# Performance work log

Measured on AMD Instinct MI355X. Metric: run time of the kernel, lower is better.

## Reference

```python
import jax, jax.numpy as jnp
import numpy as np

N_NODES = 50000
N_EDGES = 800000
EPS = 1e-5


def _glorot(key, fan_in, fan_out):
    lim = np.sqrt(6.0 / (fan_in + fan_out))
    return jax.random.uniform(key, (fan_in, fan_out), jnp.float32, -lim, lim)


def setup_inputs() -> dict:
    key = jax.random.key(0)
    ks = jax.random.split(key, 16)
    x = jax.random.normal(ks[0], (N_NODES, 88), jnp.float32)
    edge_index = jax.random.randint(ks[1], (2, N_EDGES), 0, N_NODES, jnp.int64)
    dims = [(88, 70), (70, 60), (60, 50), (50, 60), (60, 70), (70, 88)]
    inp = {"x": x, "edge_index": edge_index}
    for i, (fi, fo) in enumerate(dims):
        inp[f"W{i+1}"] = _glorot(ks[2 + i], fi, fo)
        inp[f"b{i+1}"] = jnp.zeros((fo,), jnp.float32)
    # BatchNorm affine params for layers with bn: widths 70,60,60,70
    for i, w in enumerate([70, 60, 60, 70]):
        inp[f"g{i+1}"] = jnp.ones((w,), jnp.float32)
        inp[f"be{i+1}"] = jnp.zeros((w,), jnp.float32)
    return inp


def _gcn_norm(edge_index, n_nodes):
    # add self-loops, symmetric normalization: D^-1/2 (A+I) D^-1/2
    loop = jnp.arange(n_nodes, dtype=edge_index.dtype)
    src = jnp.concatenate([edge_index[0], loop])
    dst = jnp.concatenate([edge_index[1], loop])
    deg = jax.ops.segment_sum(jnp.ones_like(dst, jnp.float32), dst, num_segments=n_nodes)
    dis = jnp.where(deg > 0, jax.lax.rsqrt(deg), 0.0)
    norm = dis[src] * dis[dst]  # [E+N]
    return src, dst, norm


def _gcn(x, W, b, src, dst, norm, n_nodes):
    h = x @ W  # transform first (small out dim)
    msg = h[src] * norm[:, None]
    return jax.ops.segment_sum(msg, dst, num_segments=n_nodes) + b


def _bn(x, g, be):
    mu = jnp.mean(x, axis=0)
    var = jnp.mean(jnp.square(x - mu), axis=0)
    return g * (x - mu) * jax.lax.rsqrt(var + EPS) + be


def reference(x, edge_index, W1, b1, W2, b2, W3, b3, W4, b4, W5, b5, W6, b6,
              g1, be1, g2, be2, g3, be3, g4, be4):
    n = x.shape[0]
    src, dst, norm = _gcn_norm(edge_index, n)
    # encoder
    h = jax.nn.relu(_gcn(x, W1, b1, src, dst, norm, n))
    h = _bn(h, g1, be1)
    h = jax.nn.relu(_gcn(h, W2, b2, src, dst, norm, n))
    h = _bn(h, g2, be2)
    h = _gcn(h, W3, b3, src, dst, norm, n)
    # decoder
    h = jax.nn.relu(_gcn(h, W4, b4, src, dst, norm, n))
    h = _bn(h, g3, be3)
    h = jax.nn.relu(_gcn(h, W5, b5, src, dst, norm, n))
    h = _bn(h, g4, be4)
    h = _gcn(h, W6, b6, src, dst, norm, n)
    return h
```

## Files before the change

### kernel.cpp

```cpp
#include <hip/hip_runtime.h>
#include <hip/hip_bf16.h>

typedef unsigned int  uint_t;
typedef unsigned short ushort_t;

#define NN 50000
#define NE 800000
#define NBLK 196

static inline int cdiv(long long a, long long b) { return (int)((a + b - 1) / b); }

__device__ inline float bflo(uint_t u) { return __uint_as_float(u << 16); }
__device__ inline float bfhi(uint_t u) { return __uint_as_float(u & 0xffff0000u); }
__device__ inline uint_t packbf(float x, float y) {
    uint_t xu = __float_as_uint(x), yu = __float_as_uint(y);
    xu += 0x7fffu + ((xu >> 16) & 1u);
    yu += 0x7fffu + ((yu >> 16) & 1u);
    return (xu >> 16) | (yu & 0xffff0000u);
}
__device__ inline ushort_t packbf1(float x) {
    uint_t xu = __float_as_uint(x);
    xu += 0x7fffu + ((xu >> 16) & 1u);
    return (ushort_t)(xu >> 16);
}


__global__ void k_prep(int* __restrict__ deg, float* __restrict__ bnacc) {
    int i = blockIdx.x * blockDim.x + threadIdx.x;
    if (i < NN) deg[i] = 0;
    if (i < 768) bnacc[i] = 0.0f;
}

__global__ void k_hist(const int* __restrict__ dst, int* __restrict__ deg) {
    int e = blockIdx.x * blockDim.x + threadIdx.x;
    if (e < NE) {
        int d = dst[e];
        if ((unsigned)d < NN) atomicAdd(&deg[d], 1);
    }
}

__global__ void k_bsum(const int* __restrict__ deg, int* __restrict__ bsum) {
    __shared__ int l[256];
    int tid = threadIdx.x;
    int i = blockIdx.x * 256 + tid;
    l[tid] = (i < NN) ? deg[i] : 0;
    __syncthreads();
    for (int o = 128; o > 0; o >>= 1) {
        if (tid < o) l[tid] += l[tid + o];
        __syncthreads();
    }
    if (tid == 0) bsum[blockIdx.x] = l[0];
}

__global__ void k_bscan(const int* __restrict__ bsum, int* __restrict__ boff,
                        int* __restrict__ row_ptr) {
    __shared__ int l[256];
    int tid = threadIdx.x;
    int v = (tid < NBLK) ? bsum[tid] : 0;
    l[tid] = v;
    __syncthreads();
    for (int o = 1; o < 256; o <<= 1) {
        int t = (tid >= o) ? l[tid - o] : 0;
        __syncthreads();
        l[tid] += t;
        __syncthreads();
    }
    boff[tid] = l[tid] - v;
    if (tid == 255) row_ptr[NN] = l[255];
}

__global__ void k_rowptr(const int* __restrict__ deg, const int* __restrict__ boff,
                         int* __restrict__ row_ptr, int* __restrict__ cursor,
                         float* __restrict__ dis) {
    __shared__ int l[256];
    int tid = threadIdx.x;
    int i = blockIdx.x * 256 + tid;
    int v = (i < NN) ? deg[i] : 0;
    l[tid] = v;
    __syncthreads();
    for (int o = 1; o < 256; o <<= 1) {
        int t = (tid >= o) ? l[tid - o] : 0;
        __syncthreads();
        l[tid] += t;
        __syncthreads();
    }
    if (i < NN) {
        int excl = boff[blockIdx.x] + l[tid] - v;
        row_ptr[i] = excl;
        cursor[i] = excl;
        dis[i] = rsqrtf((float)(v + 1));
    }
}

__global__ void k_fill(const int* __restrict__ src, const int* __restrict__ dst,
                       const float* __restrict__ dis,
                       int* __restrict__ cursor, int* __restrict__ col,
                       float* __restrict__ wgt) {
    int e = blockIdx.x * blockDim.x + threadIdx.x;
    if (e < NE) {
        int s = src[e], d = dst[e];
        if ((unsigned)s < NN && (unsigned)d < NN) {
            int p = atomicAdd(&cursor[d], 1);
            col[p] = s;
            wgt[p] = dis[s] * dis[d];
        }
    }
}

template<int FI, int FO, int IN_BN, int OUT_B>
__global__ void k_fold(const float* __restrict__ bnacc, const float* __restrict__ g,
                       const float* __restrict__ be, const float* __restrict__ b,
                       const float* __restrict__ W,
                       float* __restrict__ Wp, float* __restrict__ biasf) {
    constexpr int NT  = (FO + 15) / 16;
    constexpr int FOP = 16 * NT;
    __shared__ float scl[IN_BN ? FI : 1], shl[IN_BN ? FI : 1];
    int tid = threadIdx.x;
    if (IN_BN) {
        if (tid < FI) {
            const float inv_n = 1.0f / NN;
            float mu = bnacc[tid] * inv_n;
            float va = bnacc[96 + tid] * inv_n - mu * mu;
            float r  = rsqrtf(va + 1e-5f);
            float sc = g[tid] * r;
            scl[tid] = sc;
            shl[tid] = be[tid] - mu * sc;
        }
        __syncthreads();
    }
    for (int idx = tid; idx < FI * FOP; idx += 256) {
        int k = idx / FOP, j = idx - k * FOP;
        float w = (j < FO) ? W[k * FO + j] : 0.0f;
        if (IN_BN) w *= scl[k];
        Wp[(k >> 1) * 2 * FOP + 2 * j + (k & 1)] = w;
    }
    if (tid < FOP) {
        float a = (OUT_B && tid < FO) ? b[tid] : 0.0f;
        if (IN_BN && tid < FO) {
            #pragma unroll 4
            for (int k = 0; k < FI; ++k) a = fmaf(shl[k], W[k * FO + tid], a);
        }
        biasf[tid] = a;
    }
}

template<int FI, int FO, int IN_BN, int IN_F32, int OUT_F32>
__global__ __launch_bounds__(256)
void k_dense(const void* __restrict__ Xv, const float* __restrict__ Wp,
             const float* __restrict__ biasf, void* __restrict__ Hv) {
    constexpr int NT  = (FO + 15) / 16;
    constexpr int FOP = 16 * NT;
    constexpr int FIP = FI + 2;
    constexpr int KP  = FI / 2;

    __shared__ __align__(16) float xs[64 * FIP];

    int tid = threadIdx.x;
    int node0 = blockIdx.x * 64;

    if (IN_F32) {
        for (int idx = tid; idx < 64 * FI; idx += 256) {
            int r = idx / FI, c = idx - r * FI;
            int n = node0 + r;
            float v = (n < NN) ? ((const float*)Xv)[(size_t)n * FI + c] : 0.0f;
            if (IN_BN) v = fmaxf(v, 0.0f);
            xs[r * FIP + c] = v;
        }
    } else {
        for (int idx = tid; idx < 64 * KP; idx += 256) {
            int r = idx / KP, c2 = idx - r * KP;
            int n = node0 + r;
            uint_t u = (n < NN) ? ((const uint_t*)Xv)[(size_t)n * KP + c2] : 0u;
            float f0 = bflo(u), f1 = bfhi(u);
            if (IN_BN) { f0 = fmaxf(f0, 0.0f); f1 = fmaxf(f1, 0.0f); }
            xs[r * FIP + 2 * c2]     = f0;
            xs[r * FIP + 2 * c2 + 1] = f1;
        }
    }
    __syncthreads();

    int ng = tid >> 4;
    int cg = tid & 15;

    float acc[4][NT];
    #pragma unroll
    for (int i = 0; i < 4; ++i)
        #pragma unroll
        for (int t = 0; t < NT; ++t) acc[i][t] = biasf[cg + 16 * t];

    #pragma unroll 2
    for (int k = 0; k < FI; k += 2) {
        float2 xv[4];
        #pragma unroll
        for (int i = 0; i < 4; ++i)
            xv[i] = *(const float2*)&xs[(ng + 16 * i) * FIP + k];
        const float* wrow = &Wp[(k >> 1) * 2 * FOP];
        #pragma unroll
        for (int t = 0; t < NT; ++t) {
            float2 w = *(const float2*)&wrow[2 * (cg + 16 * t)];
            #pragma unroll
            for (int i = 0; i < 4; ++i)
                acc[i][t] = fmaf(xv[i].y, w.y, fmaf(xv[i].x, w.x, acc[i][t]));
        }
    }

    #pragma unroll
    for (int i = 0; i < 4; ++i) {
        int n = node0 + ng + 16 * i;
        if (n < NN) {
            #pragma unroll
            for (int t = 0; t < NT; ++t) {
                int j = cg + 16 * t;
                if (j < FO) {
                    if (OUT_F32) ((float*)Hv)[(size_t)n * FO + j] = acc[i][t];
                    else ((ushort_t*)Hv)[(size_t)n * FO + j] = packbf1(acc[i][t]);
                }
            }
        }
    }
}

template<int FO, int IN_BN, int OUT_BIAS>
__global__ void k_gather(const ushort_t* __restrict__ h, const int* __restrict__ row_ptr,
                         const int* __restrict__ col, const float* __restrict__ wgt,
                         const float* __restrict__ dis,
                         const float* __restrict__ bnacc, const float* __restrict__ g,
                         const float* __restrict__ be,
                         const float* __restrict__ b, ushort_t* __restrict__ A) {
    constexpr int F2 = FO / 2;
    int t = blockIdx.x * blockDim.x + threadIdx.x;
    if (t >= NN * F2) return;
    int i = t / F2;
    int j2 = t - i * F2;
    int j = 2 * j2;

    float sc0 = 1.0f, sh0 = 0.0f, sc1 = 1.0f, sh1 = 0.0f;
    if (IN_BN) {
        const float inv_n = 1.0f / NN;
        float mu0 = bnacc[j] * inv_n;
        float va0 = bnacc[96 + j] * inv_n - mu0 * mu0;
        float r0  = rsqrtf(va0 + 1e-5f);
        sc0 = g[j] * r0; sh0 = be[j] - mu0 * sc0;
        float mu1 = bnacc[j + 1] * inv_n;
        float va1 = bnacc[96 + j + 1] * inv_n - mu1 * mu1;
        float r1  = rsqrtf(va1 + 1e-5f);
        sc1 = g[j + 1] * r1; sh1 = be[j + 1] - mu1 * sc1;
    }

    const uint_t* h2 = (const uint_t*)h + j2;
    float di = dis[i];

    uint_t su = h2[(size_t)i * F2];
    float vx = bflo(su), vy = bfhi(su);
    if (IN_BN) { vx = fmaxf(vx, 0.0f) * sc0 + sh0; vy = fmaxf(vy, 0.0f) * sc1 + sh1; }
    float ax = vx * di * di;
    float ay = vy * di * di;

    int k = row_ptr[i], end = row_ptr[i + 1];
    for (; k + 8 <= end; k += 8) {
        uint_t uu[8]; float ww[8];
        #pragma unroll
        for (int q = 0; q < 8; ++q) {
            int s = col[k + q];
            ww[q] = wgt[k + q];
            uu[q] = h2[(size_t)s * F2];
        }
        #pragma unroll
        for (int q = 0; q < 8; ++q) {
            float tx = bflo(uu[q]), ty = bfhi(uu[q]);
            if (IN_BN) { tx = fmaxf(tx, 0.0f) * sc0 + sh0; ty = fmaxf(ty, 0.0f) * sc1 + sh1; }
            ax = fmaf(tx, ww[q], ax); ay = fmaf(ty, ww[q], ay);
        }
    }
    for (; k < end; ++k) {
        int s = col[k];
        float w = wgt[k];
        uint_t u = h2[(size_t)s * F2];
        float tx = bflo(u), ty = bfhi(u);
        if (IN_BN) { tx = fmaxf(tx, 0.0f) * sc0 + sh0; ty = fmaxf(ty, 0.0f) * sc1 + sh1; }
        ax = fmaf(tx, w, ax); ay = fmaf(ty, w, ay);
    }
    if (OUT_BIAS) { ax += b[j]; ay += b[j + 1]; }
    ((uint_t*)A)[(size_t)i * F2 + j2] = packbf(ax, ay);
}

template<int FO>
__global__ void k_bnpart(const ushort_t* __restrict__ A, float* __restrict__ acc) {
    constexpr int F2 = FO / 2;
    __shared__ float ls[96], lq[96];
    int tid = threadIdx.x;
    if (tid < 96) { ls[tid] = 0.0f; lq[tid] = 0.0f; }
    __syncthreads();
    const uint_t* A2 = (const uint_t*)A;
    int t2 = blockIdx.x * blockDim.x + tid;
    int j2 = t2 % F2;
    int stride = gridDim.x * blockDim.x;
    float sx = 0.0f, qx = 0.0f, sy = 0.0f, qy = 0.0f;
    for (; t2 < NN * F2; t2 += stride) {
        uint_t u = A2[t2];
        float x = fmaxf(bflo(u), 0.0f), y = fmaxf(bfhi(u), 0.0f);
        sx += x; qx += x * x;
        sy += y; qy += y * y;
    }
    atomicAdd(&ls[2 * j2], sx);     atomicAdd(&ls[2 * j2 + 1], sy);
    atomicAdd(&lq[2 * j2], qx);     atomicAdd(&lq[2 * j2 + 1], qy);
    __syncthreads();
    if (tid < FO) {
        atomicAdd(&acc[tid], ls[tid]);
        atomicAdd(&acc[96 + tid], lq[tid]);
    }
}

extern "C" void kernel_launch(void* const* d_in, const int* in_sizes, int n_in,
                              void* d_out, int out_size, void* d_ws, size_t ws_size,
                              hipStream_t stream) {
    const float* x = (const float*)d_in[0];
    const int* ei = (const int*)d_in[1];
    const int* src = ei;
    const int* dst = ei + NE;
    const float* W1 = (const float*)d_in[2];  const float* b1 = (const float*)d_in[3];
    const float* W2 = (const float*)d_in[4];  const float* b2 = (const float*)d_in[5];
    const float* W3 = (const float*)d_in[6];  const float* b3 = (const float*)d_in[7];
    const float* W4 = (const float*)d_in[8];  const float* b4 = (const float*)d_in[9];
    const float* W5 = (const float*)d_in[10]; const float* b5 = (const float*)d_in[11];
    const float* W6 = (const float*)d_in[12]; const float* b6 = (const float*)d_in[13];
    const float* g1 = (const float*)d_in[14]; const float* be1 = (const float*)d_in[15];
    const float* g2 = (const float*)d_in[16]; const float* be2 = (const float*)d_in[17];
    const float* g3 = (const float*)d_in[18]; const float* be3 = (const float*)d_in[19];
    const float* g4 = (const float*)d_in[20]; const float* be4 = (const float*)d_in[21];

    float* ws = (float*)d_ws;
    float* dis    = ws;
    float* bnacc  = dis + NN;
    float* Wp     = bnacc + 768;
    float* biasf  = Wp + 7040;
    float* wgt    = biasf + 96;
    int* deg      = (int*)(wgt + NE);
    int* row_ptr  = deg + NN;
    int* cursor   = row_ptr + NN + 1;
    int* col      = cursor + NN;
    int* bsum     = col + NE;
    int* boff     = bsum + 256;
    ushort_t* hB  = (ushort_t*)(boff + 256);
    ushort_t* aB  = hB + (size_t)NN * 70;
    float* out    = (float*)d_out;

    const int NB = 256;
    const int DGRID = cdiv(NN, 64);
    float* bn0 = bnacc;
    float* bn1 = bnacc + 192;
    float* bn2 = bnacc + 384;
    float* bn3 = bnacc + 576;

    k_prep<<<cdiv(NN, NB), NB, 0, stream>>>(deg, bnacc);
    k_hist<<<cdiv(NE, NB), NB, 0, stream>>>(dst, deg);
    k_bsum<<<NBLK, 256, 0, stream>>>(deg, bsum);
    k_bscan<<<1, 256, 0, stream>>>(bsum, boff, row_ptr);
    k_rowptr<<<NBLK, 256, 0, stream>>>(deg, boff, row_ptr, cursor, dis);
    k_fill<<<cdiv(NE, NB), NB, 0, stream>>>(src, dst, dis, cursor, col, wgt);

    k_fold<88, 70, 0, 0><<<1, 256, 0, stream>>>(nullptr, nullptr, nullptr, nullptr, W1, Wp, biasf);
    k_dense<88, 70, 0, 1, 0><<<DGRID, 256, 0, stream>>>(x, Wp, biasf, hB);
    k_gather<70, 0, 1><<<cdiv((long long)NN * 35, NB), NB, 0, stream>>>(
        hB, row_ptr, col, wgt, dis, nullptr, nullptr, nullptr, b1, aB);
    k_bnpart<70><<<35 * 56, NB, 0, stream>>>(aB, bn0);

    k_fold<70, 60, 1, 0><<<1, 256, 0, stream>>>(bn0, g1, be1, nullptr, W2, Wp, biasf);
    k_dense<70, 60, 1, 0, 0><<<DGRID, 256, 0, stream>>>(aB, Wp, biasf, hB);
    k_gather<60, 0, 1><<<cdiv((long long)NN * 30, NB), NB, 0, stream>>>(
        hB, row_ptr, col, wgt, dis, nullptr, nullptr, nullptr, b2, aB);
    k_bnpart<60><<<30 * 56, NB, 0, stream>>>(aB, bn1);

    k_fold<60, 50, 1, 0><<<1, 256, 0, stream>>>(bn1, g2, be2, nullptr, W3, Wp, biasf);
    k_dense<60, 50, 1, 0, 0><<<DGRID, 256, 0, stream>>>(aB, Wp, biasf, hB);
    k_gather<50, 0, 1><<<cdiv((long long)NN * 25, NB), NB, 0, stream>>>(
        hB, row_ptr, col, wgt, dis, nullptr, nullptr, nullptr, b3, aB);

    k_gather<50, 0, 0><<<cdiv((long long)NN * 25, NB), NB, 0, stream>>>(
        aB, row_ptr, col, wgt, dis, nullptr, nullptr, nullptr, nullptr, hB);
    k_fold<50, 60, 0, 1><<<1, 256, 0, stream>>>(nullptr, nullptr, nullptr, b4, W4, Wp, biasf);
    k_dense<50, 60, 0, 0, 0><<<DGRID, 256, 0, stream>>>(hB, Wp, biasf, aB);
    k_bnpart<60><<<30 * 56, NB, 0, stream>>>(aB, bn2);

    k_gather<60, 1, 0><<<cdiv((long long)NN * 30, NB), NB, 0, stream>>>(
        aB, row_ptr, col, wgt, dis, bn2, g3, be3, nullptr, hB);
    k_fold<60, 70, 0, 1><<<1, 256, 0, stream>>>(nullptr, nullptr, nullptr, b5, W5, Wp, biasf);
    k_dense<60, 70, 0, 0, 0><<<DGRID, 256, 0, stream>>>(hB, Wp, biasf, aB);
    k_bnpart<70><<<35 * 56, NB, 0, stream>>>(aB, bn3);

    k_gather<70, 1, 0><<<cdiv((long long)NN * 35, NB), NB, 0, stream>>>(
        aB, row_ptr, col, wgt, dis, bn3, g4, be4, nullptr, hB);
    k_fold<70, 88, 0, 1><<<1, 256, 0, stream>>>(nullptr, nullptr, nullptr, b6, W6, Wp, biasf);
    k_dense<70, 88, 0, 0, 1><<<DGRID, 256, 0, stream>>>(hB, Wp, biasf, out);
}
```

Before: 664.1 us.

## Fuse BN statistics into gather/dense, pack CSR col+weight, batch weight folds

Removes the separate k_bnpart passes by accumulating ReLU sum and sum-of-squares inside the gather or dense kernel that produces each activation. Column index and edge weight are packed into one int2 array so each edge needs a single load. The weight folds that do not depend on BN are batched into one multi-block launch at the start, and each layer gets its own Wp/bias slot. The gather becomes grid-stride with a fixed grid of 56*F2 blocks where stats are fused, which cuts parallelism and may add per-element overhead.

```diff
diff --git a/kernel.cpp b/kernel.cpp
--- a/kernel.cpp
+++ b/kernel.cpp
@@ -94,69 +94,77 @@
 
 __global__ void k_fill(const int* __restrict__ src, const int* __restrict__ dst,
                        const float* __restrict__ dis,
-                       int* __restrict__ cursor, int* __restrict__ col,
-                       float* __restrict__ wgt) {
+                       int* __restrict__ cursor, int2* __restrict__ cw) {
     int e = blockIdx.x * blockDim.x + threadIdx.x;
     if (e < NE) {
         int s = src[e], d = dst[e];
         if ((unsigned)s < NN && (unsigned)d < NN) {
             int p = atomicAdd(&cursor[d], 1);
-            col[p] = s;
-            wgt[p] = dis[s] * dis[d];
-        }
-    }
-}
-
-template<int FI, int FO, int IN_BN, int OUT_B>
-__global__ void k_fold(const float* __restrict__ bnacc, const float* __restrict__ g,
-                       const float* __restrict__ be, const float* __restrict__ b,
-                       const float* __restrict__ W,
-                       float* __restrict__ Wp, float* __restrict__ biasf) {
-    constexpr int NT  = (FO + 15) / 16;
-    constexpr int FOP = 16 * NT;
-    __shared__ float scl[IN_BN ? FI : 1], shl[IN_BN ? FI : 1];
-    int tid = threadIdx.x;
-    if (IN_BN) {
+            cw[p] = make_int2(s, __float_as_int(dis[s] * dis[d]));
+        }
+    }
+}
+
+struct FoldJob {
+    const float* W; const float* b;
+    const float* bnacc; const float* g; const float* be;
+    float* Wp; float* bf;
+    int FI, FO, in_bn, out_b;
+};
+struct FoldJobs { FoldJob j[4]; };
+
+__global__ void k_fold(FoldJobs jobs) {
+    FoldJob J = jobs.j[blockIdx.x];
+    const int FI = J.FI, FO = J.FO;
+    const int NT = (FO + 15) / 16, FOP = 16 * NT;
+    __shared__ float scl[96], shl[96];
+    int tid = threadIdx.x;
+    if (J.in_bn) {
         if (tid < FI) {
             const float inv_n = 1.0f / NN;
-            float mu = bnacc[tid] * inv_n;
-            float va = bnacc[96 + tid] * inv_n - mu * mu;
+            float mu = J.bnacc[tid] * inv_n;
+            float va = J.bnacc[96 + tid] * inv_n - mu * mu;
             float r  = rsqrtf(va + 1e-5f);
-            float sc = g[tid] * r;
+            float sc = J.g[tid] * r;
             scl[tid] = sc;
-            shl[tid] = be[tid] - mu * sc;
+            shl[tid] = J.be[tid] - mu * sc;
         }
         __syncthreads();
     }
     for (int idx = tid; idx < FI * FOP; idx += 256) {
         int k = idx / FOP, j = idx - k * FOP;
-        float w = (j < FO) ? W[k * FO + j] : 0.0f;
-        if (IN_BN) w *= scl[k];
-        Wp[(k >> 1) * 2 * FOP + 2 * j + (k & 1)] = w;
+        float w = (j < FO) ? J.W[k * FO + j] : 0.0f;
+        if (J.in_bn) w *= scl[k];
+        J.Wp[(k >> 1) * 2 * FOP + 2 * j + (k & 1)] = w;
     }
     if (tid < FOP) {
-        float a = (OUT_B && tid < FO) ? b[tid] : 0.0f;
-        if (IN_BN && tid < FO) {
-            #pragma unroll 4
-            for (int k = 0; k < FI; ++k) a = fmaf(shl[k], W[k * FO + tid], a);
-        }
-        biasf[tid] = a;
-    }
-}
-
-template<int FI, int FO, int IN_BN, int IN_F32, int OUT_F32>
+        float a = (J.out_b && tid < FO) ? J.b[tid] : 0.0f;
+        if (J.in_bn && tid < FO) {
+            for (int k = 0; k < FI; ++k) a = fmaf(shl[k], J.W[k * FO + tid], a);
+        }
+        J.bf[tid] = a;
+    }
+}
+
+template<int FI, int FO, int IN_BN, int IN_F32, int OUT_F32, int OUT_BN>
 __global__ __launch_bounds__(256)
 void k_dense(const void* __restrict__ Xv, const float* __restrict__ Wp,
-             const float* __restrict__ biasf, void* __restrict__ Hv) {
+             const float* __restrict__ biasf, void* __restrict__ Hv,
+             float* __restrict__ bnst) {
     constexpr int NT  = (FO + 15) / 16;
     constexpr int FOP = 16 * NT;
     constexpr int FIP = FI + 2;
     constexpr int KP  = FI / 2;
 
     __shared__ __align__(16) float xs[64 * FIP];
+    __shared__ float ls[96], lq[96];
 
     int tid = threadIdx.x;
     int node0 = blockIdx.x * 64;
+
+    if (OUT_BN) {
+        if (tid < 96) { ls[tid] = 0.0f; lq[tid] = 0.0f; }
+    }
 
     if (IN_F32) {
         for (int idx = tid; idx < 64 * FI; idx += 256) {
@@ -204,6 +212,27 @@
         }
     }
 
+    if (OUT_BN) {
+        #pragma unroll
+        for (int t = 0; t < NT; ++t) {
+            float ps = 0.0f, pq = 0.0f;
+            #pragma unroll
+            for (int i = 0; i < 4; ++i) {
+                if (node0 + ng + 16 * i < NN) {
+                    float r = fmaxf(acc[i][t], 0.0f);
+                    ps += r; pq += r * r;
+                }
+            }
+            atomicAdd(&ls[cg + 16 * t], ps);
+            atomicAdd(&lq[cg + 16 * t], pq);
+        }
+        __syncthreads();
+        if (tid < FO) {
+            atomicAdd(&bnst[tid], ls[tid]);
+            atomicAdd(&bnst[96 + tid], lq[tid]);
+        }
+    }
+
     #pragma unroll
     for (int i = 0; i < 4; ++i) {
         int n = node0 + ng + 16 * i;
@@ -220,18 +249,24 @@
     }
 }
 
-template<int FO, int IN_BN, int OUT_BIAS>
+template<int FO, int IN_BN, int OUT_BIAS, int OUT_BN>
 __global__ void k_gather(const ushort_t* __restrict__ h, const int* __restrict__ row_ptr,
-                         const int* __restrict__ col, const float* __restrict__ wgt,
-                         const float* __restrict__ dis,
+                         const int2* __restrict__ cw, const float* __restrict__ dis,
                          const float* __restrict__ bnacc, const float* __restrict__ g,
                          const float* __restrict__ be,
-                         const float* __restrict__ b, ushort_t* __restrict__ A) {
+                         const float* __restrict__ b, ushort_t* __restrict__ A,
+                         float* __restrict__ bnacc_out) {
     constexpr int F2 = FO / 2;
-    int t = blockIdx.x * blockDim.x + threadIdx.x;
-    if (t >= NN * F2) return;
-    int i = t / F2;
-    int j2 = t - i * F2;
+    __shared__ float ls[96], lq[96];
+    int tid = threadIdx.x;
+    if (OUT_BN) {
+        if (tid < 96) { ls[tid] = 0.0f; lq[tid] = 0.0f; }
+        __syncthreads();
+    }
+
+    int t0 = blockIdx.x * blockDim.x + tid;
+    const int stride = gridDim.x * blockDim.x;
+    int j2 = t0 % F2;
     int j = 2 * j2;
 
     float sc0 = 1.0f, sh0 = 0.0f, sc1 = 1.0f, sh1 = 0.0f;
@@ -248,66 +283,59 @@
     }
 
     const uint_t* h2 = (const uint_t*)h + j2;
-    float di = dis[i];
-
-    uint_t su = h2[(size_t)i * F2];
-    float vx = bflo(su), vy = bfhi(su);
-    if (IN_BN) { vx = fmaxf(vx, 0.0f) * sc0 + sh0; vy = fmaxf(vy, 0.0f) * sc1 + sh1; }
-    float ax = vx * di * di;
-    float ay = vy * di * di;
-
-    int k = row_ptr[i], end = row_ptr[i + 1];
-    for (; k + 8 <= end; k += 8) {
-        uint_t uu[8]; float ww[8];
-        #pragma unroll
-        for (int q = 0; q < 8; ++q) {
-            int s = col[k + q];
-            ww[q] = wgt[k + q];
-            uu[q] = h2[(size_t)s * F2];
-        }
-        #pragma unroll
-        for (int q = 0; q < 8; ++q) {
-            float tx = bflo(uu[q]), ty = bfhi(uu[q]);
+    float sx = 0.0f, qx = 0.0f, sy = 0.0f, qy = 0.0f;
+
+    for (int t = t0; t < NN * F2; t += stride) {
+        int i = t / F2;
+        float di = dis[i];
+
+        uint_t su = h2[(size_t)i * F2];
+        float vx = bflo(su), vy = bfhi(su);
+        if (IN_BN) { vx = fmaxf(vx, 0.0f) * sc0 + sh0; vy = fmaxf(vy, 0.0f) * sc1 + sh1; }
+        float ax = vx * di * di;
+        float ay = vy * di * di;
+
+        int k = row_ptr[i], end = row_ptr[i + 1];
+        for (; k + 8 <= end; k += 8) {
+            uint_t uu[8]; float ww[8];
+            #pragma unroll
+            for (int q = 0; q < 8; ++q) {
+                int2 c = cw[k + q];
+                ww[q] = __int_as_float(c.y);
+                uu[q] = h2[(size_t)c.x * F2];
+            }
+            #pragma unroll
+            for (int q = 0; q < 8; ++q) {
+                float tx = bflo(uu[q]), ty = bfhi(uu[q]);
+                if (IN_BN) { tx = fmaxf(tx, 0.0f) * sc0 + sh0; ty = fmaxf(ty, 0.0f) * sc1 + sh1; }
+                ax = fmaf(tx, ww[q], ax); ay = fmaf(ty, ww[q], ay);
+            }
+        }
+        for (; k < end; ++k) {
+            int2 c = cw[k];
+            float w = __int_as_float(c.y);
+            uint_t u = h2[(size_t)c.x * F2];
+            float tx = bflo(u), ty = bfhi(u);
             if (IN_BN) { tx = fmaxf(tx, 0.0f) * sc0 + sh0; ty = fmaxf(ty, 0.0f) * sc1 + sh1; }
-            ax = fmaf(tx, ww[q], ax); ay = fmaf(ty, ww[q], ay);
-        }
-    }
-    for (; k < end; ++k) {
-        int s = col[k];
-        float w = wgt[k];
-        uint_t u = h2[(size_t)s * F2];
-        float tx = bflo(u), ty = bfhi(u);
-        if (IN_BN) { tx = fmaxf(tx, 0.0f) * sc0 + sh0; ty = fmaxf(ty, 0.0f) * sc1 + sh1; }
-        ax = fmaf(tx, w, ax); ay = fmaf(ty, w, ay);
-    }
-    if (OUT_BIAS) { ax += b[j]; ay += b[j + 1]; }
-    ((uint_t*)A)[(size_t)i * F2 + j2] = packbf(ax, ay);
-}
-
-template<int FO>
-__global__ void k_bnpart(const ushort_t* __restrict__ A, float* __restrict__ acc) {
-    constexpr int F2 = FO / 2;
-    __shared__ float ls[96], lq[96];
-    int tid = threadIdx.x;
-    if (tid < 96) { ls[tid] = 0.0f; lq[tid] = 0.0f; }
-    __syncthreads();
-    const uint_t* A2 = (const uint_t*)A;
-    int t2 = blockIdx.x * blockDim.x + tid;
-    int j2 = t2 % F2;
-    int stride = gridDim.x * blockDim.x;
-    float sx = 0.0f, qx = 0.0f, sy = 0.0f, qy = 0.0f;
-    for (; t2 < NN * F2; t2 += stride) {
-        uint_t u = A2[t2];
-        float x = fmaxf(bflo(u), 0.0f), y = fmaxf(bfhi(u), 0.0f);
-        sx += x; qx += x * x;
-        sy += y; qy += y * y;
-    }
-    atomicAdd(&ls[2 * j2], sx);     atomicAdd(&ls[2 * j2 + 1], sy);
-    atomicAdd(&lq[2 * j2], qx);     atomicAdd(&lq[2 * j2 + 1], qy);
-    __syncthreads();
-    if (tid < FO) {
-        atomicAdd(&acc[tid], ls[tid]);
-        atomicAdd(&acc[96 + tid], lq[tid]);
+            ax = fmaf(tx, w, ax); ay = fmaf(ty, w, ay);
+        }
+        if (OUT_BIAS) { ax += b[j]; ay += b[j + 1]; }
+        if (OUT_BN) {
+            float rx = fmaxf(ax, 0.0f), ry = fmaxf(ay, 0.0f);
+            sx += rx; qx += rx * rx;
+            sy += ry; qy += ry * ry;
+        }
+        ((uint_t*)A)[(size_t)i * F2 + j2] = packbf(ax, ay);
+    }
+
+    if (OUT_BN) {
+        atomicAdd(&ls[j], sx);     atomicAdd(&ls[j + 1], sy);
+        atomicAdd(&lq[j], qx);     atomicAdd(&lq[j + 1], qy);
+        __syncthreads();
+        if (tid < FO) {
+            atomicAdd(&bnacc_out[tid], ls[tid]);
+            atomicAdd(&bnacc_out[96 + tid], lq[tid]);
+        }
     }
 }
 
@@ -333,13 +361,12 @@
     float* dis    = ws;
     float* bnacc  = dis + NN;
     float* Wp     = bnacc + 768;
-    float* biasf  = Wp + 7040;
-    float* wgt    = biasf + 96;
-    int* deg      = (int*)(wgt + NE);
+    float* biasf  = Wp + 6 * 7040;
+    int2* cw      = (int2*)(biasf + 6 * 96);
+    int* deg      = (int*)(cw + NE);
     int* row_ptr  = deg + NN;
     int* cursor   = row_ptr + NN + 1;
-    int* col      = cursor + NN;
-    int* bsum     = col + NE;
+    int* bsum     = cursor + NN;
     int* boff     = bsum + 256;
     ushort_t* hB  = (ushort_t*)(boff + 256);
     ushort_t* aB  = hB + (size_t)NN * 70;
@@ -351,45 +378,56 @@
     float* bn1 = bnacc + 192;
     float* bn2 = bnacc + 384;
     float* bn3 = bnacc + 576;
+    float* WpL[6]; float* bfL[6];
+    for (int i = 0; i < 6; ++i) { WpL[i] = Wp + i * 7040; bfL[i] = biasf + i * 96; }
 
     k_prep<<<cdiv(NN, NB), NB, 0, stream>>>(deg, bnacc);
     k_hist<<<cdiv(NE, NB), NB, 0, stream>>>(dst, deg);
     k_bsum<<<NBLK, 256, 0, stream>>>(deg, bsum);
     k_bscan<<<1, 256, 0, stream>>>(bsum, boff, row_ptr);
     k_rowptr<<<NBLK, 256, 0, stream>>>(deg, boff, row_ptr, cursor, dis);
-    k_fill<<<cdiv(NE, NB), NB, 0, stream>>>(src, dst, dis, cursor, col, wgt);
-
-    k_fold<88, 70, 0, 0><<<1, 256, 0, stream>>>(nullptr, nullptr, nullptr, nullptr, W1, Wp, biasf);
-    k_dense<88, 70, 0, 1, 0><<<DGRID, 256, 0, stream>>>(x, Wp, biasf, hB);
-    k_gather<70, 0, 1><<<cdiv((long long)NN * 35, NB), NB, 0, stream>>>(
-        hB, row_ptr, col, wgt, dis, nullptr, nullptr, nullptr, b1, aB);
-    k_bnpart<70><<<35 * 56, NB, 0, stream>>>(aB, bn0);
-
-    k_fold<70, 60, 1, 0><<<1, 256, 0, stream>>>(bn0, g1, be1, nullptr, W2, Wp, biasf);
-    k_dense<70, 60, 1, 0, 0><<<DGRID, 256, 0, stream>>>(aB, Wp, biasf, hB);
-    k_gather<60, 0, 1><<<cdiv((long long)NN * 30, NB), NB, 0, stream>>>(
-        hB, row_ptr, col, wgt, dis, nullptr, nullptr, nullptr, b2, aB);
-    k_bnpart<60><<<30 * 56, NB, 0, stream>>>(aB, bn1);
-
-    k_fold<60, 50, 1, 0><<<1, 256, 0, stream>>>(bn1, g2, be2, nullptr, W3, Wp, biasf);
-    k_dense<60, 50, 1, 0, 0><<<DGRID, 256, 0, stream>>>(aB, Wp, biasf, hB);
-    k_gather<50, 0, 1><<<cdiv((long long)NN * 25, NB), NB, 0, stream>>>(
-        hB, row_ptr, col, wgt, dis, nullptr, nullptr, nullptr, b3, aB);
-
-    k_gather<50, 0, 0><<<cdiv((long long)NN * 25, NB), NB, 0, stream>>>(
-        aB, row_ptr, col, wgt, dis, nullptr, nullptr, nullptr, nullptr, hB);
-    k_fold<50, 60, 0, 1><<<1, 256, 0, stream>>>(nullptr, nullptr, nullptr, b4, W4, Wp, biasf);
-    k_dense<50, 60, 0, 0, 0><<<DGRID, 256, 0, stream>>>(hB, Wp, biasf, aB);
-    k_bnpart<60><<<30 * 56, NB, 0, stream>>>(aB, bn2);
-
-    k_gather<60, 1, 0><<<cdiv((long long)NN * 30, NB), NB, 0, stream>>>(
-        aB, row_ptr, col, wgt, dis, bn2, g3, be3, nullptr, hB);
-    k_fold<60, 70, 0, 1><<<1, 256, 0, stream>>>(nullptr, nullptr, nullptr, b5, W5, Wp, biasf);
-    k_dense<60, 70, 0, 0, 0><<<DGRID, 256, 0, stream>>>(hB, Wp, biasf, aB);
-    k_bnpart<70><<<35 * 56, NB, 0, stream>>>(aB, bn3);
-
-    k_gather<70, 1, 0><<<cdiv((long long)NN * 35, NB), NB, 0, stream>>>(
-        aB, row_ptr, col, wgt, dis, bn3, g4, be4, nullptr, hB);
-    k_fold<70, 88, 0, 1><<<1, 256, 0, stream>>>(nullptr, nullptr, nullptr, b6, W6, Wp, biasf);
-    k_dense<70, 88, 0, 0, 1><<<DGRID, 256, 0, stream>>>(hB, Wp, biasf, out);
-}
+    k_fill<<<cdiv(NE, NB), NB, 0, stream>>>(src, dst, dis, cursor, cw);
+
+    {
+        FoldJobs js;
+        js.j[0] = {W1, nullptr, nullptr, nullptr, nullptr, WpL[0], bfL[0], 88, 70, 0, 0};
+        js.j[1] = {W4, b4,      nullptr, nullptr, nullptr, WpL[3], bfL[3], 50, 60, 0, 1};
+        js.j[2] = {W5, b5,      nullptr, nullptr, nullptr, WpL[4], bfL[4], 60, 70, 0, 1};
+        js.j[3] = {W6, b6,      nullptr, nullptr, nullptr, WpL[5], bfL[5], 70, 88, 0, 1};
+        k_fold<<<4, 256, 0, stream>>>(js);
+    }
+
+    k_dense<88, 70, 0, 1, 0, 0><<<DGRID, 256, 0, stream>>>(x, WpL[0], bfL[0], hB, nullptr);
+    k_gather<70, 0, 1, 1><<<56 * 35, NB, 0, stream>>>(
+        hB, row_ptr, cw, dis, nullptr, nullptr, nullptr, b1, aB, bn0);
+
+    {
+        FoldJobs js;
+        js.j[0] = {W2, nullptr, bn0, g1, be1, WpL[1], bfL[1], 70, 60, 1, 0};
+        k_fold<<<1, 256, 0, stream>>>(js);
+    }
+    k_dense<70, 60, 1, 0, 0, 0><<<DGRID, 256, 0, stream>>>(aB, WpL[1], bfL[1], hB, nullptr);
+    k_gather<60, 0, 1, 1><<<56 * 30, NB, 0, stream>>>(
+        hB, row_ptr, cw, dis, nullptr, nullptr, nullptr, b2, aB, bn1);
+
+    {
+        FoldJobs js;
+        js.j[0] = {W3, nullptr, bn1, g2, be2, WpL[2], bfL[2], 60, 50, 1, 0};
+        k_fold<<<1, 256, 0, stream>>>(js);
+    }
+    k_dense<60, 50, 1, 0, 0, 0><<<DGRID, 256, 0, stream>>>(aB, WpL[2], bfL[2], hB, nullptr);
+    k_gather<50, 0, 1, 0><<<cdiv((long long)NN * 25, NB), NB, 0, stream>>>(
+        hB, row_ptr, cw, dis, nullptr, nullptr, nullptr, b3, aB, nullptr);
+
+    k_gather<50, 0, 0, 0><<<cdiv((long long)NN * 25, NB), NB, 0, stream>>>(
+        aB, row_ptr, cw, dis, nullptr, nullptr, nullptr, nullptr, hB, nullptr);
+    k_dense<50, 60, 0, 0, 0, 1><<<DGRID, 256, 0, stream>>>(hB, WpL[3], bfL[3], aB, bn2);
+
+    k_gather<60, 1, 0, 0><<<cdiv((long long)NN * 30, NB), NB, 0, stream>>>(
+        aB, row_ptr, cw, dis, bn2, g3, be3, nullptr, hB, nullptr);
+    k_dense<60, 70, 0, 0, 0, 1><<<DGRID, 256, 0, stream>>>(hB, WpL[4], bfL[4], aB, bn3);
+
+    k_gather<70, 1, 0, 0><<<cdiv((long long)NN * 35, NB), NB, 0, stream>>>(
+        aB, row_ptr, cw, dis, bn3, g4, be4, nullptr, hB, nullptr);
+    k_dense<70, 88, 0, 0, 1, 0><<<DGRID, 256, 0, stream>>>(hB, WpL[5], bfL[5], out, nullptr);
+}
```

New measurement: 557.3 us. 1.19x faster.
